# Kernel optimization log

Hardware: AMD Instinct MI355X
Metric: run time of the kernel (lower is better)

Reference implementation:

```python
import jax, jax.numpy as jnp
import numpy as np

D_MODEL = 1024
D_HEAD = 64
RANK = 8
LEAF = 4
NUM_LEAVES = D_HEAD // LEAF            # 16
NUM_LEVELS = 4                          # log2(64/4)
BLOCK_SIZES = [4, 8, 16, 32]
RANKS = [min(RANK, b) for b in BLOCK_SIZES]   # [4,8,8,8]
NUM_NODES = [NUM_LEAVES // 2 ** (l + 1) for l in range(NUM_LEVELS)]  # [8,4,2,1]


def _elu1(x):
    return jax.nn.elu(x) + 1.0


def setup_inputs() -> dict:
    key = jax.random.key(0)
    ks = jax.random.split(key, 32)
    B, T = 8, 2048
    x = jax.random.normal(ks[0], (B, T, D_MODEL), jnp.float32)
    s_in = 1.0 / np.sqrt(D_MODEL)
    s_out = 1.0 / np.sqrt(D_HEAD)
    inp = {
        'x': x,
        'Wq': jax.random.normal(ks[1], (D_MODEL, D_HEAD), jnp.float32) * s_in,
        'Wk': jax.random.normal(ks[2], (D_MODEL, D_HEAD), jnp.float32) * s_in,
        'Wv': jax.random.normal(ks[3], (D_MODEL, D_HEAD), jnp.float32) * s_in,
        'Wo': jax.random.normal(ks[4], (D_HEAD, D_MODEL), jnp.float32) * s_out,
    }
    # Fixed orthonormal bases per level (torch.linalg.qr of randn in original)
    idx = 5
    for name in ['UL', 'VR', 'UR', 'VL']:
        for l in range(NUM_LEVELS):
            bs, rl = BLOCK_SIZES[l], RANKS[l]
            Q, _ = jnp.linalg.qr(jax.random.normal(ks[idx], (bs, rl), jnp.float32))
            inp[f'{name}{l}'] = Q
            idx += 1
    return inp


def _hss_forward(x, Wq, Wk, Wv, Wo, UL, VR, UR, VL):
    B, T, _ = x.shape
    q = _elu1(x @ Wq)   # (B,T,Dh)
    k = _elu1(x @ Wk)
    v = x @ Wv

    leaf0 = jnp.zeros((B, NUM_LEAVES, LEAF, LEAF), x.dtype)
    Ws0 = tuple(jnp.zeros((B, NUM_NODES[l], RANKS[l], RANKS[l]), x.dtype)
                for l in range(NUM_LEVELS))
    z0 = jnp.zeros((B, D_HEAD), x.dtype)

    def step(carry, kvq):
        leaf, Ws, z = carry
        k_t, v_t, q_t = kvq  # each (B, Dh)
        # rank-1 update: leaf diagonal blocks
        leaf = leaf + jnp.einsum('bni,bnj->bnij',
                                 k_t.reshape(B, NUM_LEAVES, LEAF),
                                 v_t.reshape(B, NUM_LEAVES, LEAF))
        newWs = []
        for l in range(NUM_LEVELS):
            bs, nn = BLOCK_SIZES[l], NUM_NODES[l]
            u_r = k_t.reshape(B, nn, 2 * bs)
            v_r = v_t.reshape(B, nn, 2 * bs)
            uL = jnp.einsum('bnd,dr->bnr', u_r[:, :, :bs], UL[l])
            vR = jnp.einsum('bnd,dr->bnr', v_r[:, :, bs:], VR[l])
            newWs.append(Ws[l] + jnp.einsum('bni,bnj->bnij', uL, vR))
        Ws = tuple(newWs)
        z = z + k_t
        # HSS matvec: y = S @ q_t
        y = jnp.einsum('bnij,bnj->bni', leaf,
                       q_t.reshape(B, NUM_LEAVES, LEAF)).reshape(B, D_HEAD)
        for l in range(NUM_LEVELS):
            bs, nn = BLOCK_SIZES[l], NUM_NODES[l]
            x_r = q_t.reshape(B, nn, 2 * bs)
            vr_x = jnp.einsum('bnd,dr->bnr', x_r[:, :, bs:], VR[l])
            y_top = jnp.einsum('dr,bnr->bnd', UL[l],
                               jnp.einsum('bnij,bnj->bni', Ws[l], vr_x))
            vl_x = jnp.einsum('bnd,dr->bnr', x_r[:, :, :bs], VL[l])
            y_bot = jnp.einsum('dr,bnr->bnd', UR[l],
                               jnp.einsum('bnji,bnj->bni', Ws[l], vl_x))
            y = y + jnp.concatenate([y_top, y_bot], axis=-1).reshape(B, D_HEAD)
        denom = jnp.maximum(jnp.sum(z * q_t, axis=-1, keepdims=True), 1e-6)
        return (leaf, Ws, z), y / denom

    kvq = (jnp.swapaxes(k, 0, 1), jnp.swapaxes(v, 0, 1), jnp.swapaxes(q, 0, 1))
    _, outs = jax.lax.scan(step, (leaf0, Ws0, z0), kvq)  # (T,B,Dh)
    out = jnp.swapaxes(outs, 0, 1)  # (B,T,Dh); dropout is identity in eval
    return out @ Wo


def reference(x, Wq, Wk, Wv, Wo,
              UL0, UL1, UL2, UL3,
              VR0, VR1, VR2, VR3,
              UR0, UR1, UR2, UR3,
              VL0, VL1, VL2, VL3):
    UL = (UL0, UL1, UL2, UL3)
    VR = (VR0, VR1, VR2, VR3)
    UR = (UR0, UR1, UR2, UR3)
    VL = (VL0, VL1, VL2, VL3)
    return _hss_forward(x, Wq, Wk, Wv, Wo, UL, VR, UR, VL)
```

## Files before the change

### kernel.cpp

```cpp
#include <hip/hip_runtime.h>
#include <hip/hip_bf16.h>

typedef unsigned short u16;
typedef __attribute__((ext_vector_type(8))) short bf16x8;
typedef __attribute__((ext_vector_type(4))) float f32x4;

#define B_ 8
#define T_ 2048
#define BT_ (B_*T_)
#define DM_ 1024
#define DH_ 64
#define NCH_ 64
#define S_ (T_/NCH_)
#define STATE_ 896

__device__ __forceinline__ float b2f(u16 u){ unsigned v=((unsigned)u)<<16; float f; __builtin_memcpy(&f,&v,4); return f; }
__device__ __forceinline__ u16 f2b(float f){ __hip_bfloat16 h=__float2bfloat16(f); u16 u; __builtin_memcpy(&u,&h,2); return u; }

__device__ __forceinline__ float ldin(const void* p, size_t i, int f32){
  return f32 ? ((const float*)p)[i] : b2f(((const u16*)p)[i]);
}
__device__ __forceinline__ bf16x8 ld8bf(const void* p, size_t i, int f32){
  if (f32){
    f32x4 v0 = *(const f32x4*)((const float*)p + i);
    f32x4 v1 = *(const f32x4*)((const float*)p + i + 4);
    bf16x8 r;
    #pragma unroll
    for (int j=0;j<4;j++){ r[j] = (short)f2b(v0[j]); r[4+j] = (short)f2b(v1[j]); }
    return r;
  }
  return *(const bf16x8*)((const u16*)p + i);
}

__device__ __forceinline__ void decodeWs(int e, int& ia, int& ib){
  if (e<384){ int o=e-256, n=o>>4; ia=n*4+((o>>2)&3); ib=n*4+(o&3); }
  else if (e<640){ int o=e-384, n=o>>6; ia=32+n*8+((o>>3)&7); ib=32+n*8+(o&7); }
  else if (e<768){ int o=e-640, n=o>>6; ia=64+n*8+((o>>3)&7); ib=64+n*8+(o&7); }
  else { int o=e-768; ia=80+((o>>3)&7); ib=80+(o&7); }
}
__device__ __forceinline__ void decode88(int f, int& l, int& n, int& ri){
  if (f<32){ l=0; n=f>>2; ri=f&3; }
  else if (f<64){ l=1; n=(f-32)>>3; ri=f&7; }
  else if (f<80){ l=2; n=(f-64)>>3; ri=f&7; }
  else { l=3; n=0; ri=f&7; }
}

__global__ __launch_bounds__(64) void k_detect(const u16* __restrict__ x, int* __restrict__ flag){
  int tid = threadIdx.x;
  int sane = 0;
  for (int i = tid; i < 4096; i += 64){
    u16 u = x[i];
    int e = (u >> 7) & 0xFF;
    if ((u & 0x7FFF) == 0 || (e >= 100 && e <= 140)) sane++;
  }
  #pragma unroll
  for (int o = 32; o > 0; o >>= 1) sane += __shfl_down(sane, o);
  if (tid == 0) flag[0] = (sane < 3600) ? 1 : 0;
}

__global__ __launch_bounds__(256) void k_wfrag(
    const void* __restrict__ Wq, const void* __restrict__ Wk, const void* __restrict__ Wv,
    const void* __restrict__ Wo,
    const void* __restrict__ UL0, const void* __restrict__ UL1, const void* __restrict__ UL2, const void* __restrict__ UL3,
    const void* __restrict__ VR0, const void* __restrict__ VR1, const void* __restrict__ VR2, const void* __restrict__ VR3,
    const void* __restrict__ VL0, const void* __restrict__ VL1, const void* __restrict__ VL2, const void* __restrict__ VL3,
    u16* __restrict__ WF, u16* __restrict__ WoF, u16* __restrict__ PF,
    const int* __restrict__ fl)
{
  const int f32 = fl[0];
  int e = blockIdx.x*256 + threadIdx.x;
  if (e < 24576){
    int m = e >> 13;
    int rem = e & 8191;
    int ks = rem >> 8;
    int nt = (rem >> 6) & 3;
    int lane = rem & 63;
    const void* W = (m==0)?Wq:((m==1)?Wk:Wv);
    int kr = ks*32 + (lane>>4)*8;
    int col = nt*16 + (lane&15);
    u16 o[8];
    #pragma unroll
    for (int j=0;j<8;j++) o[j] = f2b(ldin(W, (size_t)(kr+j)*DH_ + col, f32));
    u16* dst = WF + (size_t)e*8;
    #pragma unroll
    for (int j=0;j<8;j++) dst[j] = o[j];
  } else if (e < 32768){
    int eo = e - 24576;
    int ks = eo >> 12;
    int nt = (eo >> 6) & 63;
    int lane = eo & 63;
    int kr = ks*32 + (lane>>4)*8;
    int col = nt*16 + (lane&15);
    u16 o[8];
    #pragma unroll
    for (int j=0;j<8;j++) o[j] = f2b(ldin(Wo, (size_t)(kr+j)*DM_ + col, f32));
    u16* dst = WoF + (size_t)eo*8;
    #pragma unroll
    for (int j=0;j<8;j++) dst[j] = o[j];
  } else if (e < 35072){
    int pe = e - 32768;
    int lane = pe & 63;
    int nt = (pe >> 6) % 6;
    int mk = pe / 384;
    int ks = mk & 1, mat = mk >> 1;
    int col = nt*16 + (lane&15);
    int dbase = ks*32 + (lane>>4)*8;
    const int BSl[4]={4,8,16,32}; const int Rl[4]={4,8,8,8};
    u16 o[8];
    #pragma unroll
    for (int j=0;j<8;j++){
      float val = 0.f;
      if (col < 88){
        int l,n,ri; decode88(col,l,n,ri);
        int bs=BSl[l], r=Rl[l];
        int lo = n*2*bs + ((mat==1)?bs:0);
        int d = dbase + j;
        if (d >= lo && d < lo+bs){
          const void* Up;
          if (mat==0)      Up = (l==0)?UL0:(l==1)?UL1:(l==2)?UL2:UL3;
          else if (mat==1) Up = (l==0)?VR0:(l==1)?VR1:(l==2)?VR2:VR3;
          else             Up = (l==0)?VL0:(l==1)?VL1:(l==2)?VL2:VL3;
          val = ldin(Up, (size_t)(d-lo)*r + ri, f32);
        }
      }
      o[j] = f2b(val);
    }
    u16* dst = PF + (size_t)pe*8;
    #pragma unroll
    for (int j=0;j<8;j++) dst[j] = o[j];
  }
}

__global__ __launch_bounds__(768, 8) void k_proj5(
    const void* __restrict__ x, const u16* __restrict__ WF,
    float* __restrict__ oq, float* __restrict__ ok_, float* __restrict__ ov,
    u16* __restrict__ qb16, u16* __restrict__ kb16, u16* __restrict__ vb16,
    const int* __restrict__ fl)
{
  __shared__ f32x4 red[9][4][64];
  const int f32 = fl[0];
  const int rows0 = blockIdx.x*16;
  const int wv = threadIdx.x>>6;
  const int m  = wv>>2;
  const int kq = wv&3;
  const int lane = threadIdx.x&63;
  const int quad = lane>>4, l16 = lane&15;
  const size_t rowA = (size_t)(rows0 + l16)*DM_;

  f32x4 acc[4];
  #pragma unroll
  for (int i=0;i<4;i++) acc[i] = (f32x4){0.f,0.f,0.f,0.f};

  const int ks0 = kq*8;
  #pragma unroll 2
  for (int kk=0;kk<8;kk++){
    int ks = ks0 + kk;
    int ko = ks*32 + quad*8;
    bf16x8 a = ld8bf(x, rowA + ko, f32);
    #pragma unroll
    for (int nt=0;nt<4;nt++){
      bf16x8 b = *(const bf16x8*)(WF + ((size_t)((m*32+ks)*4+nt)*64 + lane)*8);
      acc[nt] = __builtin_amdgcn_mfma_f32_16x16x32_bf16(a,b,acc[nt],0,0,0);
    }
  }

  if (kq>0){
    #pragma unroll
    for (int i=0;i<4;i++) red[m*3+(kq-1)][i][lane] = acc[i];
  }
  __syncthreads();
  if (kq==0){
    #pragma unroll
    for (int i=0;i<4;i++){
      f32x4 r0 = red[m*3+0][i][lane];
      f32x4 r1 = red[m*3+1][i][lane];
      f32x4 r2 = red[m*3+2][i][lane];
      acc[i][0]+=r0[0]+r1[0]+r2[0]; acc[i][1]+=r0[1]+r1[1]+r2[1];
      acc[i][2]+=r0[2]+r1[2]+r2[2]; acc[i][3]+=r0[3]+r1[3]+r2[3];
    }
    float* __restrict__ outp = (m==0)?oq:((m==1)?ok_:ov);
    u16* __restrict__ outb = (m==0)?qb16:((m==1)?kb16:vb16);
    #pragma unroll
    for (int nt=0;nt<4;nt++){
      #pragma unroll
      for (int i=0;i<4;i++){
        int row = rows0 + quad*4 + i;
        int col = nt*16 + l16;
        float val = acc[nt][i];
        if (m<2) val = (val>0.f)? (val+1.f) : expf(val);
        outp[(size_t)row*DH_ + col] = val;
        outb[(size_t)row*DH_ + col] = f2b(val);
      }
    }
  }
}

__global__ __launch_bounds__(64) void k_prep3(
    const u16* __restrict__ qb16, const u16* __restrict__ kb16, const u16* __restrict__ vb16,
    const u16* __restrict__ PF,
    float* __restrict__ uLa, float* __restrict__ vRa, float* __restrict__ vrxa, float* __restrict__ vlxa)
{
  const int m = blockIdx.y;
  const int rows0 = blockIdx.x*16;
  const int lane = threadIdx.x;
  const int quad = lane>>4, l16 = lane&15;

  const u16* __restrict__ src = (m==0)?kb16:((m==1)?vb16:qb16);
  const int mat = (m==0)?0:((m==3)?2:1);

  bf16x8 a[2];
  #pragma unroll
  for (int ks=0;ks<2;ks++){
    size_t off = (size_t)(rows0 + l16)*DH_ + ks*32 + quad*8;
    a[ks] = *(const bf16x8*)(src + off);
  }
  f32x4 acc[6];
  #pragma unroll
  for (int nt=0;nt<6;nt++) acc[nt] = (f32x4){0.f,0.f,0.f,0.f};

  #pragma unroll
  for (int ks=0;ks<2;ks++){
    #pragma unroll
    for (int nt=0;nt<6;nt++){
      bf16x8 b = *(const bf16x8*)(PF + ((size_t)((mat*2+ks)*6+nt)*64 + lane)*8);
      acc[nt] = __builtin_amdgcn_mfma_f32_16x16x32_bf16(a[ks], b, acc[nt],0,0,0);
    }
  }
  float* __restrict__ dst = (m==0)?uLa:(m==1)?vRa:(m==2)?vrxa:vlxa;
  #pragma unroll
  for (int nt=0;nt<6;nt++){
    int col = nt*16 + l16;
    if (col < 88){
      #pragma unroll
      for (int i=0;i<4;i++){
        int row = rows0 + quad*4 + i;
        dst[(size_t)row*88 + col] = acc[nt][i];
      }
    }
  }
}

__global__ __launch_bounds__(256) void k_chunksum(
    const float* __restrict__ gk, const float* __restrict__ gv,
    const float* __restrict__ uLa, const float* __restrict__ vRa,
    float* __restrict__ SL)
{
  const int bid = blockIdx.x;
  const int b = bid/NCH_, c = bid%NCH_;
  const size_t base64 = (size_t)(b*T_ + c*S_)*64;
  const size_t base88 = (size_t)(b*T_ + c*S_)*88;
  for (int p=0;p<4;p++){
    int e = threadIdx.x + p*256;
    if (e>=STATE_) break;
    float acc=0.f;
    if (e < 256){
      int n=e>>4;
      const float* A = gk + base64 + n*4 + ((e>>2)&3);
      const float* Bp = gv + base64 + n*4 + (e&3);
      for (int s=0;s<S_;s++) acc += A[s*64]*Bp[s*64];
    } else if (e < 832){
      int ia, ib; decodeWs(e, ia, ib);
      const float* A = uLa + base88 + ia;
      const float* Bp = vRa + base88 + ib;
      for (int s=0;s<S_;s++) acc += A[s*88]*Bp[s*88];
    } else {
      const float* A = gk + base64 + (e-832);
      for (int s=0;s<S_;s++) acc += A[s*64];
    }
    SL[(size_t)bid*STATE_ + e] = acc;
  }
}

__global__ __launch_bounds__(256) void k_prefix(const float* __restrict__ SL, float* __restrict__ SP){
  const int b = blockIdx.x;
  for (int p=0;p<4;p++){
    int e = threadIdx.x + p*256;
    if (e>=STATE_) break;
    float run=0.f;
    for (int c=0;c<NCH_;c++){
      size_t idx = ((size_t)(b*NCH_+c))*STATE_ + e;
      SP[idx] = run; run += SL[idx];
    }
  }
}

__global__ __launch_bounds__(256) void k_intra(
    const float* __restrict__ gq, const float* __restrict__ gk, const float* __restrict__ gv,
    const float* __restrict__ uLa, const float* __restrict__ vRa,
    const float* __restrict__ vrxa, const float* __restrict__ vlxa,
    const float* __restrict__ SP,
    const void* __restrict__ UL0, const void* __restrict__ UL1, const void* __restrict__ UL2, const void* __restrict__ UL3,
    const void* __restrict__ UR0, const void* __restrict__ UR1, const void* __restrict__ UR2, const void* __restrict__ UR3,
    u16* __restrict__ Yb, const int* __restrict__ fl)
{
  __shared__ float kS[S_*64];
  __shared__ float vS[S_*64];
  __shared__ float uvS[S_*176];
  __shared__ float st0[STATE_];
  __shared__ float ULs[464], URs[464];
  const int f32 = fl[0];
  const int tid = threadIdx.x;
  const int bid = blockIdx.x;
  const int b = bid/NCH_, c = bid%NCH_;
  const int row0 = b*T_ + c*S_;

  const size_t r64 = (size_t)row0*64;
  for (int i=tid;i<S_*64;i+=256){ kS[i]=gk[r64+i]; vS[i]=gv[r64+i]; }
  const size_t r88 = (size_t)row0*88;
  for (int i=tid;i<S_*88;i+=256){
    int s=i/88, f=i-s*88;
    uvS[s*176+f]    = uLa[r88+i];
    uvS[s*176+88+f] = vRa[r88+i];
  }
  for (int e=tid;e<STATE_;e+=256) st0[e] = SP[(size_t)bid*STATE_+e];
  for (int e=tid;e<464;e+=256){
    int l, idx;
    if (e<16){ l=0; idx=e; } else if (e<80){ l=1; idx=e-16; }
    else if (e<208){ l=2; idx=e-80; } else { l=3; idx=e-208; }
    const void* ul = (l==0)?UL0:(l==1)?UL1:(l==2)?UL2:UL3;
    const void* ur = (l==0)?UR0:(l==1)?UR1:(l==2)?UR2:UR3;
    ULs[e] = ldin(ul, idx, f32); URs[e] = ldin(ur, idx, f32);
  }
  __syncthreads();

  const int w = tid>>6, lane = tid&63, tl = lane>>3, g = lane&7;
  const int t = w*8 + tl;
  const int n1 = g>>1, ri1 = (g&1)*4;
  const int n2 = g>>2, ri2 = (g&3)*2;
  const size_t row = (size_t)(row0 + t);

  float qr[8];
  { const float* qp = gq + row*64 + g*8;
    *(f32x4*)&qr[0] = *(const f32x4*)qp; *(f32x4*)&qr[4] = *(const f32x4*)(qp+4); }
  float rxL0[4], lxL0[4], rxL1[8], lxL1[8], rxL2[8], lxL2[8], rxL3[8], lxL3[8];
  { const float* rp = vrxa + row*88; const float* lp = vlxa + row*88;
    *(f32x4*)&rxL0[0] = *(const f32x4*)(rp + 4*g);
    *(f32x4*)&lxL0[0] = *(const f32x4*)(lp + 4*g);
    *(f32x4*)&rxL1[0] = *(const f32x4*)(rp + 32 + n1*8); *(f32x4*)&rxL1[4] = *(const f32x4*)(rp + 36 + n1*8);
    *(f32x4*)&lxL1[0] = *(const f32x4*)(lp + 32 + n1*8); *(f32x4*)&lxL1[4] = *(const f32x4*)(lp + 36 + n1*8);
    *(f32x4*)&rxL2[0] = *(const f32x4*)(rp + 64 + n2*8); *(f32x4*)&rxL2[4] = *(const f32x4*)(rp + 68 + n2*8);
    *(f32x4*)&lxL2[0] = *(const f32x4*)(lp + 64 + n2*8); *(f32x4*)&lxL2[4] = *(const f32x4*)(lp + 68 + n2*8);
    *(f32x4*)&rxL3[0] = *(const f32x4*)(rp + 80); *(f32x4*)&rxL3[4] = *(const f32x4*)(rp + 84);
    *(f32x4*)&lxL3[0] = *(const f32x4*)(lp + 80); *(f32x4*)&lxL3[4] = *(const f32x4*)(lp + 84); }

  float yacc[8], den = 0.f;
  #pragma unroll
  for (int cc=0;cc<8;cc++){
    int n = 2*g + (cc>>2);
    const float* m = &st0[n*16 + (cc&3)*4];
    const float* qp = &qr[(cc>>2)*4];
    yacc[cc] = m[0]*qp[0]+m[1]*qp[1]+m[2]*qp[2]+m[3]*qp[3];
    den += st0[832 + g*8 + cc]*qr[cc];
  }
  float gtL0[4], gbL0[4], gtL1[4], gbL1[4], gtL2[2], gbL2[2], gtL3, gbL3;
  #pragma unroll
  for (int cc=0;cc<4;cc++){
    const float* m = &st0[256 + g*16 + cc*4];
    gtL0[cc] = m[0]*rxL0[0]+m[1]*rxL0[1]+m[2]*rxL0[2]+m[3]*rxL0[3];
    float s2 = 0.f;
    #pragma unroll
    for (int j=0;j<4;j++) s2 += st0[256 + g*16 + j*4 + cc]*lxL0[j];
    gbL0[cc] = s2;
  }
  #pragma unroll
  for (int cc=0;cc<4;cc++){
    int ri = ri1 + cc;
    float s1=0.f, s2=0.f;
    #pragma unroll
    for (int j=0;j<8;j++){
      s1 += st0[384 + n1*64 + ri*8 + j]*rxL1[j];
      s2 += st0[384 + n1*64 + j*8 + ri]*lxL1[j];
    }
    gtL1[cc]=s1; gbL1[cc]=s2;
  }
  #pragma unroll
  for (int cc=0;cc<2;cc++){
    int ri = ri2 + cc;
    float s1=0.f, s2=0.f;
    #pragma unroll
    for (int j=0;j<8;j++){
      s1 += st0[640 + n2*64 + ri*8 + j]*rxL2[j];
      s2 += st0[640 + n2*64 + j*8 + ri]*lxL2[j];
    }
    gtL2[cc]=s1; gbL2[cc]=s2;
  }
  { float s1=0.f, s2=0.f;
    #pragma unroll
    for (int j=0;j<8;j++){
      s1 += st0[768 + g*8 + j]*rxL3[j];
      s2 += st0[768 + j*8 + g]*lxL3[j];
    }
    gtL3=s1; gbL3=s2; }

  const int smax = w*8 + 8;
  for (int s=0; s<smax; s++){
    const float* ks_ = &kS[s*64 + g*8];
    const float* vs_ = &vS[s*64 + g*8];
    const float* uL_ = &uvS[s*176];
    const float* vR_ = &uvS[s*176 + 88];
    float dv0 = vs_[0]*qr[0]+vs_[1]*qr[1]+vs_[2]*qr[2]+vs_[3]*qr[3];
    float dv1 = vs_[4]*qr[4]+vs_[5]*qr[5]+vs_[6]*qr[6]+vs_[7]*qr[7];
    float dn = 0.f;
    #pragma unroll
    for (int cc=0;cc<8;cc++) dn += ks_[cc]*qr[cc];
    float d1L0=0.f,d2L0=0.f;
    #pragma unroll
    for (int j=0;j<4;j++){ d1L0 += vR_[4*g+j]*rxL0[j]; d2L0 += uL_[4*g+j]*lxL0[j]; }
    float d1L1=0.f,d2L1=0.f;
    #pragma unroll
    for (int j=0;j<8;j++){ d1L1 += vR_[32+n1*8+j]*rxL1[j]; d2L1 += uL_[32+n1*8+j]*lxL1[j]; }
    float d1L2=0.f,d2L2=0.f;
    #pragma unroll
    for (int j=0;j<8;j++){ d1L2 += vR_[64+n2*8+j]*rxL2[j]; d2L2 += uL_[64+n2*8+j]*lxL2[j]; }
    float d1L3=0.f,d2L3=0.f;
    #pragma unroll
    for (int j=0;j<8;j++){ d1L3 += vR_[80+j]*rxL3[j]; d2L3 += uL_[80+j]*lxL3[j]; }
    if (s<=t){
      den += dn;
      #pragma unroll
      for (int cc=0;cc<8;cc++) yacc[cc] += ks_[cc]*((cc<4)?dv0:dv1);
      #pragma unroll
      for (int cc=0;cc<4;cc++){
        gtL0[cc] += uL_[4*g+cc]*d1L0;          gbL0[cc] += vR_[4*g+cc]*d2L0;
        gtL1[cc] += uL_[32+n1*8+ri1+cc]*d1L1;  gbL1[cc] += vR_[32+n1*8+ri1+cc]*d2L1;
      }
      #pragma unroll
      for (int cc=0;cc<2;cc++){
        gtL2[cc] += uL_[64+n2*8+ri2+cc]*d1L2;  gbL2[cc] += vR_[64+n2*8+ri2+cc]*d2L2;
      }
      gtL3 += uL_[80+g]*d1L3;  gbL3 += vR_[80+g]*d2L3;
    }
  }
  __syncthreads();

  { float* gr = &uvS[t*176];
    #pragma unroll
    for (int cc=0;cc<4;cc++){
      gr[4*g+cc] = gtL0[cc];                 gr[88+4*g+cc] = gbL0[cc];
      gr[32+n1*8+ri1+cc] = gtL1[cc];         gr[88+32+n1*8+ri1+cc] = gbL1[cc];
    }
    #pragma unroll
    for (int cc=0;cc<2;cc++){
      gr[64+n2*8+ri2+cc] = gtL2[cc];         gr[88+64+n2*8+ri2+cc] = gbL2[cc];
    }
    gr[80+g] = gtL3;  gr[88+80+g] = gbL3;
  }
  __syncthreads();

  den += __shfl_xor(den,1); den += __shfl_xor(den,2); den += __shfl_xor(den,4);
  float inv = 1.f / fmaxf(den, 1e-6f);
  const float* gr = &uvS[t*176];
  float yout[8];
  #pragma unroll
  for (int cc=0;cc<8;cc++){
    int j = g*8 + cc;
    float y = yacc[cc];
    if (cc<4){
      #pragma unroll
      for (int rr=0;rr<4;rr++) y += ULs[cc*4+rr]*gr[g*4+rr];
    } else {
      #pragma unroll
      for (int rr=0;rr<4;rr++) y += URs[(cc-4)*4+rr]*gr[88+g*4+rr];
    }
    { int seg=j>>4, pos=j&15;
      if (pos<8){
        #pragma unroll
        for (int rr=0;rr<8;rr++) y += ULs[16+pos*8+rr]*gr[32+seg*8+rr];
      } else {
        #pragma unroll
        for (int rr=0;rr<8;rr++) y += URs[16+(pos-8)*8+rr]*gr[88+32+seg*8+rr];
      } }
    { int seg=j>>5, pos=j&31;
      if (pos<16){
        #pragma unroll
        for (int rr=0;rr<8;rr++) y += ULs[80+pos*8+rr]*gr[64+seg*8+rr];
      } else {
        #pragma unroll
        for (int rr=0;rr<8;rr++) y += URs[80+(pos-16)*8+rr]*gr[88+64+seg*8+rr];
      } }
    { int pos=j;
      if (pos<32){
        #pragma unroll
        for (int rr=0;rr<8;rr++) y += ULs[208+pos*8+rr]*gr[80+rr];
      } else {
        #pragma unroll
        for (int rr=0;rr<8;rr++) y += URs[208+(pos-32)*8+rr]*gr[88+80+rr];
      } }
    yout[cc] = y*inv;
  }
  u16* yp = Yb + row*64 + g*8;
  ushort4 o1, o2;
  o1.x=f2b(yout[0]); o1.y=f2b(yout[1]); o1.z=f2b(yout[2]); o1.w=f2b(yout[3]);
  o2.x=f2b(yout[4]); o2.y=f2b(yout[5]); o2.z=f2b(yout[6]); o2.w=f2b(yout[7]);
  *(ushort4*)yp = o1;
  *(ushort4*)(yp+4) = o2;
}

__global__ __launch_bounds__(64,4) void k_outproj3(
    const u16* __restrict__ Yb, const u16* __restrict__ WoF, void* __restrict__ outv,
    const int* __restrict__ fl)
{
  const int f32 = fl[0];
  const int rows0 = blockIdx.x*32;
  const int nt0 = blockIdx.y*8;
  const int lane = threadIdx.x;
  const int quad = lane>>4, l16 = lane&15;

  f32x4 acc[16];
  #pragma unroll
  for (int i=0;i<16;i++) acc[i] = (f32x4){0.f,0.f,0.f,0.f};

  #pragma unroll
  for (int ks=0;ks<2;ks++){
    int ko = ks*32 + quad*8;
    bf16x8 a0 = *(const bf16x8*)(Yb + (size_t)(rows0 + l16)*DH_ + ko);
    bf16x8 a1 = *(const bf16x8*)(Yb + (size_t)(rows0 + 16 + l16)*DH_ + ko);
    #pragma unroll
    for (int nt=0;nt<8;nt++){
      bf16x8 b = *(const bf16x8*)(WoF + ((size_t)(ks*64 + nt0 + nt)*64 + lane)*8);
      acc[nt]   = __builtin_amdgcn_mfma_f32_16x16x32_bf16(a0,b,acc[nt],0,0,0);
      acc[8+nt] = __builtin_amdgcn_mfma_f32_16x16x32_bf16(a1,b,acc[8+nt],0,0,0);
    }
  }
  #pragma unroll
  for (int sp=0;sp<2;sp++){
    #pragma unroll
    for (int nt=0;nt<8;nt++){
      #pragma unroll
      for (int i=0;i<4;i++){
        int row = rows0 + sp*16 + quad*4 + i;
        int col = (nt0+nt)*16 + l16;
        size_t idx = (size_t)row*DM_ + col;
        float v = acc[sp*8+nt][i];
        if (f32) ((float*)outv)[idx] = v;
        else ((u16*)outv)[idx] = f2b(v);
      }
    }
  }
}

extern "C" void kernel_launch(void* const* d_in, const int* in_sizes, int n_in,
                              void* d_out, int out_size, void* d_ws, size_t ws_size,
                              hipStream_t stream) {
  const void* x  = d_in[0];
  const void* Wq = d_in[1];
  const void* Wk = d_in[2];
  const void* Wv = d_in[3];
  const void* Wo = d_in[4];
  const void* UL[4] = {d_in[5],d_in[6],d_in[7],d_in[8]};
  const void* VR[4] = {d_in[9],d_in[10],d_in[11],d_in[12]};
  const void* UR[4] = {d_in[13],d_in[14],d_in[15],d_in[16]};
  const void* VL[4] = {d_in[17],d_in[18],d_in[19],d_in[20]};

  int* flag = (int*)d_ws;
  float* ws = (float*)d_ws + 16;
  float* q    = ws;
  float* kf   = q    + (size_t)BT_*64;
  float* vf   = kf   + (size_t)BT_*64;
  float* uLa  = vf   + (size_t)BT_*64;
  float* vRa  = uLa  + (size_t)BT_*88;
  float* vrxa = vRa  + (size_t)BT_*88;
  float* vlxa = vrxa + (size_t)BT_*88;
  float* SL   = vlxa + (size_t)BT_*88;
  float* SP   = SL   + (size_t)B_*NCH_*STATE_;
  u16*   Yb   = (u16*)(SP + (size_t)B_*NCH_*STATE_);
  u16*   WF   = Yb  + (size_t)BT_*64;
  u16*   WoF  = WF  + (size_t)196608;
  u16*   PF   = WoF + (size_t)65536;
  u16*   qb16 = PF  + (size_t)18432;
  u16*   kb16 = qb16 + (size_t)BT_*64;
  u16*   vb16 = kb16 + (size_t)BT_*64;

  k_detect<<<1, 64, 0, stream>>>((const u16*)x, flag);
  k_wfrag<<<137, 256, 0, stream>>>(Wq, Wk, Wv, Wo,
      UL[0],UL[1],UL[2],UL[3], VR[0],VR[1],VR[2],VR[3], VL[0],VL[1],VL[2],VL[3],
      WF, WoF, PF, flag);
  k_proj5<<<BT_/16, 768, 0, stream>>>(x, WF, q, kf, vf, qb16, kb16, vb16, flag);
  k_prep3<<<dim3(BT_/16, 4), 64, 0, stream>>>(qb16, kb16, vb16, PF, uLa, vRa, vrxa, vlxa);
  k_chunksum<<<B_*NCH_, 256, 0, stream>>>(kf, vf, uLa, vRa, SL);
  k_prefix<<<B_, 256, 0, stream>>>(SL, SP);
  k_intra<<<B_*NCH_, 256, 0, stream>>>(q, kf, vf, uLa, vRa, vrxa, vlxa, SP,
      UL[0],UL[1],UL[2],UL[3], UR[0],UR[1],UR[2],UR[3], Yb, flag);
  k_outproj3<<<dim3(512, 8), 64, 0, stream>>>(Yb, WoF, d_out, flag);
}
```

Measured before the change: 278.2 us.

## Restructure QKV projection to 64-row tiles with LDS-staged weights

The QKV projection kernel now processes 64 rows per block (4 row groups x 2 K-halves) instead of 16, with each wave computing all 12 output fragments for q, k and v. Weight fragments are staged into LDS via global_load_lds with double buffering, so one weight load is shared by four row groups. This cuts redundant weight traffic and makes the split-K reduction two-way. In exchange it needs a barrier every K step, more accumulator registers, and fewer blocks (256), which could reduce occupancy and latency hiding.

```diff
diff --git a/kernel.cpp b/kernel.cpp
--- a/kernel.cpp
+++ b/kernel.cpp
@@ -30,6 +30,11 @@
     return r;
   }
   return *(const bf16x8*)((const u16*)p + i);
+}
+
+__device__ __forceinline__ void gl_lds16(const void* g, void* l){
+  __builtin_amdgcn_global_load_lds((const __attribute__((address_space(1))) unsigned int*)g,
+                                   (__attribute__((address_space(3))) unsigned int*)l, 16, 0, 0);
 }
 
 __device__ __forceinline__ void decodeWs(int e, int& ia, int& ib){
@@ -131,65 +136,90 @@
   }
 }
 
-__global__ __launch_bounds__(768, 8) void k_proj5(
+__global__ __launch_bounds__(512, 4) void k_proj7(
     const void* __restrict__ x, const u16* __restrict__ WF,
     float* __restrict__ oq, float* __restrict__ ok_, float* __restrict__ ov,
     u16* __restrict__ qb16, u16* __restrict__ kb16, u16* __restrict__ vb16,
     const int* __restrict__ fl)
 {
-  __shared__ f32x4 red[9][4][64];
+  __shared__ __align__(16) char sh[49152];
   const int f32 = fl[0];
-  const int rows0 = blockIdx.x*16;
-  const int wv = threadIdx.x>>6;
-  const int m  = wv>>2;
-  const int kq = wv&3;
-  const int lane = threadIdx.x&63;
+  const int tid = threadIdx.x;
+  const int wv = tid>>6;
+  const int mg = wv>>1;
+  const int h  = wv&1;
+  const int lane = tid&63;
   const int quad = lane>>4, l16 = lane&15;
+  const int rows0 = blockIdx.x*64 + mg*16;
   const size_t rowA = (size_t)(rows0 + l16)*DM_;
 
-  f32x4 acc[4];
-  #pragma unroll
-  for (int i=0;i<4;i++) acc[i] = (f32x4){0.f,0.f,0.f,0.f};
-
-  const int ks0 = kq*8;
-  #pragma unroll 2
-  for (int kk=0;kk<8;kk++){
-    int ks = ks0 + kk;
-    int ko = ks*32 + quad*8;
-    bf16x8 a = ld8bf(x, rowA + ko, f32);
-    #pragma unroll
-    for (int nt=0;nt<4;nt++){
-      bf16x8 b = *(const bf16x8*)(WF + ((size_t)((m*32+ks)*4+nt)*64 + lane)*8);
-      acc[nt] = __builtin_amdgcn_mfma_f32_16x16x32_bf16(a,b,acc[nt],0,0,0);
-    }
-  }
-
-  if (kq>0){
-    #pragma unroll
-    for (int i=0;i<4;i++) red[m*3+(kq-1)][i][lane] = acc[i];
-  }
+  f32x4 acc[12];
+  #pragma unroll
+  for (int i=0;i<12;i++) acc[i] = (f32x4){0.f,0.f,0.f,0.f};
+
+  #define STAGE(t, buf) do{                                                   \
+    _Pragma("unroll")                                                         \
+    for (int r=0;r<3;r++){                                                    \
+      int s = wv + r*8;                                                       \
+      int hs = (s>=12) ? 1 : 0;                                               \
+      int f = s - hs*12;                                                      \
+      int m_ = f>>2, nt_ = f&3;                                               \
+      int ks_ = hs*16 + (t);                                                  \
+      const char* src = (const char*)WF + (size_t)((m_*32+ks_)*4+nt_)*1024 + (size_t)lane*16; \
+      char* dst = sh + (buf)*24576 + hs*12288 + f*1024 + lane*16;             \
+      gl_lds16(src, dst);                                                     \
+    } }while(0)
+
+  STAGE(0, 0);
+  bf16x8 a_cur = ld8bf(x, rowA + (size_t)(h*16)*32 + quad*8, f32);
+  asm volatile("s_waitcnt vmcnt(0)" ::: "memory");
   __syncthreads();
-  if (kq==0){
-    #pragma unroll
-    for (int i=0;i<4;i++){
-      f32x4 r0 = red[m*3+0][i][lane];
-      f32x4 r1 = red[m*3+1][i][lane];
-      f32x4 r2 = red[m*3+2][i][lane];
-      acc[i][0]+=r0[0]+r1[0]+r2[0]; acc[i][1]+=r0[1]+r1[1]+r2[1];
-      acc[i][2]+=r0[2]+r1[2]+r2[2]; acc[i][3]+=r0[3]+r1[3]+r2[3];
-    }
-    float* __restrict__ outp = (m==0)?oq:((m==1)?ok_:ov);
-    u16* __restrict__ outb = (m==0)?qb16:((m==1)?kb16:vb16);
-    #pragma unroll
-    for (int nt=0;nt<4;nt++){
-      #pragma unroll
-      for (int i=0;i<4;i++){
-        int row = rows0 + quad*4 + i;
-        int col = nt*16 + l16;
-        float val = acc[nt][i];
-        if (m<2) val = (val>0.f)? (val+1.f) : expf(val);
-        outp[(size_t)row*DH_ + col] = val;
-        outb[(size_t)row*DH_ + col] = f2b(val);
+
+  bf16x8 a_nxt = a_cur;
+  for (int t=0;t<16;t++){
+    int buf = t&1;
+    if (t<15){
+      STAGE(t+1, buf^1);
+      a_nxt = ld8bf(x, rowA + (size_t)(h*16+t+1)*32 + quad*8, f32);
+    }
+    const char* bb = sh + buf*24576 + h*12288;
+    #pragma unroll
+    for (int f=0;f<12;f++){
+      bf16x8 b = *(const bf16x8*)(bb + f*1024 + lane*16);
+      acc[f] = __builtin_amdgcn_mfma_f32_16x16x32_bf16(a_cur, b, acc[f],0,0,0);
+    }
+    a_cur = a_nxt;
+    asm volatile("s_waitcnt vmcnt(0)" ::: "memory");
+    __syncthreads();
+  }
+  #undef STAGE
+
+  if (h==1){
+    #pragma unroll
+    for (int i=0;i<12;i++) ((f32x4*)sh)[(mg*12+i)*64 + lane] = acc[i];
+  }
+  __syncthreads();
+  if (h==0){
+    #pragma unroll
+    for (int i=0;i<12;i++){
+      f32x4 r = ((f32x4*)sh)[(mg*12+i)*64 + lane];
+      acc[i][0]+=r[0]; acc[i][1]+=r[1]; acc[i][2]+=r[2]; acc[i][3]+=r[3];
+    }
+    #pragma unroll
+    for (int m=0;m<3;m++){
+      float* __restrict__ outp = (m==0)?oq:((m==1)?ok_:ov);
+      u16* __restrict__ outb = (m==0)?qb16:((m==1)?kb16:vb16);
+      #pragma unroll
+      for (int nt=0;nt<4;nt++){
+        #pragma unroll
+        for (int i=0;i<4;i++){
+          int row = rows0 + quad*4 + i;
+          int col = nt*16 + l16;
+          float val = acc[m*4+nt][i];
+          if (m<2) val = (val>0.f)? (val+1.f) : expf(val);
+          outp[(size_t)row*DH_ + col] = val;
+          outb[(size_t)row*DH_ + col] = f2b(val);
+        }
       }
     }
   }
@@ -575,7 +605,7 @@
   k_wfrag<<<137, 256, 0, stream>>>(Wq, Wk, Wv, Wo,
       UL[0],UL[1],UL[2],UL[3], VR[0],VR[1],VR[2],VR[3], VL[0],VL[1],VL[2],VL[3],
       WF, WoF, PF, flag);
-  k_proj5<<<BT_/16, 768, 0, stream>>>(x, WF, q, kf, vf, qb16, kb16, vb16, flag);
+  k_proj7<<<BT_/64, 512, 0, stream>>>(x, WF, q, kf, vf, qb16, kb16, vb16, flag);
   k_prep3<<<dim3(BT_/16, 4), 64, 0, stream>>>(qb16, kb16, vb16, PF, uLa, vRa, vrxa, vlxa);
   k_chunksum<<<B_*NCH_, 256, 0, stream>>>(kf, vf, uLa, vRa, SL);
   k_prefix<<<B_, 256, 0, stream>>>(SL, SP);
```

New measurement: 265.7 us. 4.5% less time.
